# Kernel tuning notes

Measured on AMD Instinct MI355X. Metric: run time of the kernel, lower is better.

Reference implementation:

```python
import jax, jax.numpy as jnp
import numpy as np

NUM_GRAPHS = 100  # batch of graphs for pooling (dgl.max_nodes / WeightAndSum)


def _glorot(k, shape):
    lim = np.sqrt(6.0 / (shape[0] + shape[1])).astype(np.float32)
    return jax.random.uniform(k, shape, jnp.float32, -lim, lim)


def setup_inputs() -> dict:
    key = jax.random.key(0)
    ks = jax.random.split(key, 10)
    N, E, D, H = 100000, 1600000, 128, 128
    node_feats = jax.random.normal(ks[0], (N, D), dtype=jnp.float32)
    src = jax.random.randint(ks[1], (E,), 0, N, dtype=jnp.int32)
    dst = jax.random.randint(ks[2], (E,), 0, N, dtype=jnp.int32)
    graph_ids = jnp.sort(jax.random.randint(ks[3], (N,), 0, NUM_GRAPHS, dtype=jnp.int32))
    W1 = _glorot(ks[4], (D, H)); b1 = jnp.zeros((H,), jnp.float32)
    W2 = _glorot(ks[5], (H, H)); b2 = jnp.zeros((H,), jnp.float32)
    W3 = _glorot(ks[6], (H, H)); b3 = jnp.zeros((H,), jnp.float32)
    W_pool = _glorot(ks[7], (H, 1)); b_pool = jnp.zeros((1,), jnp.float32)
    return {"node_feats": node_feats, "src": src, "dst": dst, "graph_ids": graph_ids,
            "W1": W1, "b1": b1, "W2": W2, "b2": b2, "W3": W3, "b3": b3,
            "W_pool": W_pool, "b_pool": b_pool}


def _gcn_layer(h, W, b, src, dst, norm_src, norm_dst, N):
    # DGL GraphConv, norm='both': D_dst^{-1/2} (A^T (D_src^{-1/2} X W)) + b
    h = (h * norm_src[:, None]) @ W                      # [N, H]
    agg = jax.ops.segment_sum(h[src], dst, num_segments=N)  # gather + scatter-add
    return agg * norm_dst[:, None] + b


def reference(node_feats, src, dst, graph_ids, W1, b1, W2, b2, W3, b3, W_pool, b_pool):
    N = node_feats.shape[0]
    # dgl.add_self_loop (allow_zero_in_degree=False)
    loops = jnp.arange(N, dtype=src.dtype)
    src_sl = jnp.concatenate([src, loops])
    dst_sl = jnp.concatenate([dst, loops])
    ones = jnp.ones(src_sl.shape, jnp.float32)
    out_deg = jax.ops.segment_sum(ones, src_sl, num_segments=N)
    in_deg = jax.ops.segment_sum(ones, dst_sl, num_segments=N)
    norm_src = jax.lax.rsqrt(jnp.maximum(out_deg, 1.0))
    norm_dst = jax.lax.rsqrt(jnp.maximum(in_deg, 1.0))
    h = node_feats
    for W, b in ((W1, b1), (W2, b2), (W3, b3)):
        h = jax.nn.relu(_gcn_layer(h, W, b, src_sl, dst_sl, norm_src, norm_dst, N))
    # pooling_func: WeightAndSum (sigmoid-gated weighted sum per graph) + max_nodes
    w = jax.nn.sigmoid(h @ W_pool + b_pool)              # [N, 1]
    g_sum = jax.ops.segment_sum(h * w, graph_ids, num_segments=NUM_GRAPHS)
    g_max = jax.ops.segment_max(h, graph_ids, num_segments=NUM_GRAPHS)
    return jnp.concatenate([g_sum, g_max], axis=1)       # [G, 2H]
```

## Files before the change

### kernel.cpp

```cpp
#include <hip/hip_runtime.h>
#include <hip/hip_bf16.h>

#define DIM 128
#define CAP 64
#define NBMAX 64
#define BCAP 36864
#define CSPLIT 8

typedef __attribute__((ext_vector_type(8))) short bf16x8;
typedef __attribute__((ext_vector_type(4))) float f32x4;
typedef __bf16 bf16x2 __attribute__((ext_vector_type(2)));
union U16 { uint4 u; bf16x8 b; };
union UB { unsigned u; bf16x2 h; };

__device__ __forceinline__ unsigned short f2bf(float f) {
    unsigned u = __float_as_uint(f);
    unsigned r = (u + 0x7fffu + ((u >> 16) & 1u)) >> 16;
    return (unsigned short)r;
}
__device__ __forceinline__ unsigned pack2bf(float a, float b) {
    return (unsigned)f2bf(a) | ((unsigned)f2bf(b) << 16);
}
__device__ __forceinline__ float2 unpack2bf(unsigned v) {
    float2 r;
    r.x = __uint_as_float(v << 16);
    r.y = __uint_as_float(v & 0xffff0000u);
    return r;
}
__device__ __forceinline__ void accum8s(float* acc, uint4 v, float s) {
    float2 f0 = unpack2bf(v.x), f1 = unpack2bf(v.y);
    float2 f2 = unpack2bf(v.z), f3 = unpack2bf(v.w);
    acc[0] += s * f0.x; acc[1] += s * f0.y; acc[2] += s * f1.x; acc[3] += s * f1.y;
    acc[4] += s * f2.x; acc[5] += s * f2.y; acc[6] += s * f3.x; acc[7] += s * f3.y;
}
__device__ __forceinline__ void accum8m(float* acc, uint4 v, float s) {
    UB w0, w1, w2, w3;
    w0.u = v.x; w1.u = v.y; w2.u = v.z; w3.u = v.w;
    acc[0] = fmaf((float)w0.h[0], s, acc[0]);
    acc[1] = fmaf((float)w0.h[1], s, acc[1]);
    acc[2] = fmaf((float)w1.h[0], s, acc[2]);
    acc[3] = fmaf((float)w1.h[1], s, acc[3]);
    acc[4] = fmaf((float)w2.h[0], s, acc[4]);
    acc[5] = fmaf((float)w2.h[1], s, acc[5]);
    acc[6] = fmaf((float)w3.h[0], s, acc[6]);
    acc[7] = fmaf((float)w3.h[1], s, acc[7]);
}

__global__ __launch_bounds__(256) void k_bin(const int* __restrict__ src,
                                             const int* __restrict__ dst, int E,
                                             unsigned* __restrict__ binD,
                                             unsigned short* __restrict__ binS,
                                             int* __restrict__ cntD,
                                             int* __restrict__ cntS, int NB, int binGrid,
                                             const float* __restrict__ W1,
                                             const float* __restrict__ W2,
                                             const float* __restrict__ W3,
                                             unsigned* __restrict__ wT1g,
                                             unsigned* __restrict__ wT2g,
                                             unsigned* __restrict__ wT3g) {
    __shared__ int hD[NBMAX], hS[NBMAX], bD[NBMAX], bS[NBMAX];
    int t = threadIdx.x;
    if ((int)blockIdx.x >= binGrid) {
        int w = blockIdx.x - binGrid;
        const float* Wsrc = (w == 0) ? W1 : (w == 1) ? W2 : W3;
        unsigned* wTg = (w == 0) ? wT1g : (w == 1) ? wT2g : wT3g;
        int n = t >> 1;
        int kp0 = (t & 1) * 32;
#pragma unroll
        for (int i = 0; i < 32; i++) {
            int kp = kp0 + i;
            wTg[n * 64 + kp] = pack2bf(Wsrc[(2 * kp) * DIM + n], Wsrc[(2 * kp + 1) * DIM + n]);
        }
        return;
    }
    if (t < NB) { hD[t] = 0; hS[t] = 0; }
    __syncthreads();
    int e0 = blockIdx.x * 1024 + t * 4;
    int s[4], d[4];
    bool v[4];
#pragma unroll
    for (int i = 0; i < 4; i++) {
        v[i] = (e0 + i) < E;
        s[i] = 0; d[i] = 0;
        if (v[i]) { s[i] = src[e0 + i]; d[i] = dst[e0 + i]; }
    }
#pragma unroll
    for (int i = 0; i < 4; i++) {
        if (v[i]) {
            atomicAdd(&hD[d[i] >> 11], 1);
            atomicAdd(&hS[s[i] >> 11], 1);
        }
    }
    __syncthreads();
    if (t < NB) {
        bD[t] = atomicAdd(&cntD[t], hD[t]);
        bS[t] = atomicAdd(&cntS[t], hS[t]);
        hD[t] = 0; hS[t] = 0;
    }
    __syncthreads();
#pragma unroll
    for (int i = 0; i < 4; i++) {
        if (v[i]) {
            int bd = d[i] >> 11;
            int r = atomicAdd(&hD[bd], 1);
            int idx = bD[bd] + r;
            if (idx < BCAP)
                binD[bd * BCAP + idx] = ((unsigned)(d[i] & 2047) << 17) | (unsigned)s[i];
            int bs = s[i] >> 11;
            int r2 = atomicAdd(&hS[bs], 1);
            int idx2 = bS[bs] + r2;
            if (idx2 < BCAP) binS[bs * BCAP + idx2] = (unsigned short)(s[i] & 2047);
        }
    }
}

__global__ __launch_bounds__(256) void k_mega(const unsigned* __restrict__ binD,
                                              const unsigned short* __restrict__ binS,
                                              const int* __restrict__ cntD,
                                              const int* __restrict__ cntS,
                                              int* __restrict__ in_cnt,
                                              int* __restrict__ out_cnt,
                                              int* __restrict__ csr_pad,
                                              const float* __restrict__ x,
                                              const unsigned* __restrict__ wT1g,
                                              unsigned* __restrict__ xwb, int N,
                                              int NB) {
    __shared__ __align__(16) char smem[34816];
    int bid = blockIdx.x;
    int t = threadIdx.x;

    if (bid < NB * CSPLIT) {
        int b = bid / CSPLIT;
        int sub = bid - b * CSPLIT;
        int* h = (int*)smem;
        int* bArr = ((int*)smem) + 2048;
        for (int j = t; j < 2048; j += 256) h[j] = 0;
        __syncthreads();
        int base = b << 11;
        int nE = cntD[b];
        if (nE > BCAP) nE = BCAP;
        int chunk = (nE + CSPLIT - 1) / CSPLIT;
        int i0 = sub * chunk;
        int i1 = i0 + chunk;
        if (i1 > nE) i1 = nE;
        const unsigned* bb = &binD[b * BCAP];
        for (int i = i0 + t * 4; i < i1; i += 1024) {
            unsigned e[4];
            int k = i1 - i;
            if (k > 4) k = 4;
#pragma unroll
            for (int j = 0; j < 4; j++)
                if (j < k) e[j] = bb[i + j];
#pragma unroll
            for (int j = 0; j < 4; j++)
                if (j < k) atomicAdd(&h[e[j] >> 17], 1);
        }
        __syncthreads();
        for (int j = t; j < 2048; j += 256) {
            int hv = h[j];
            bArr[j] = hv ? atomicAdd(&in_cnt[base + j], hv) : 0;
            h[j] = 0;
        }
        __syncthreads();
        for (int i = i0 + t * 4; i < i1; i += 1024) {
            unsigned e[4];
            int k = i1 - i;
            if (k > 4) k = 4;
#pragma unroll
            for (int j = 0; j < 4; j++)
                if (j < k) e[j] = bb[i + j];
#pragma unroll
            for (int j = 0; j < 4; j++)
                if (j < k) {
                    int dl = (int)(e[j] >> 17);
                    int pos = bArr[dl] + atomicAdd(&h[dl], 1);
                    if (pos < CAP)
                        csr_pad[(size_t)(base + dl) * CAP + pos] = (int)(e[j] & 0x1FFFFu);
                }
        }
        return;
    }
    if (bid < 2 * NB * CSPLIT) {
        int bb2 = bid - NB * CSPLIT;
        int b = bb2 / CSPLIT;
        int sub = bb2 - b * CSPLIT;
        int* hist = (int*)smem;
        for (int j = t; j < 2048; j += 256) hist[j] = 0;
        __syncthreads();
        int base = b << 11;
        int nE = cntS[b];
        if (nE > BCAP) nE = BCAP;
        int chunk = (nE + CSPLIT - 1) / CSPLIT;
        int i0 = sub * chunk;
        int i1 = i0 + chunk;
        if (i1 > nE) i1 = nE;
        const unsigned short* bs = &binS[b * BCAP];
        for (int i = i0 + t * 4; i < i1; i += 1024) {
            unsigned short e[4];
            int k = i1 - i;
            if (k > 4) k = 4;
#pragma unroll
            for (int j = 0; j < 4; j++)
                if (j < k) e[j] = bs[i + j];
#pragma unroll
            for (int j = 0; j < 4; j++)
                if (j < k) atomicAdd(&hist[(int)e[j]], 1);
        }
        __syncthreads();
        for (int j = t; j < 2048; j += 256) {
            int hv = hist[j];
            if (hv) atomicAdd(&out_cnt[base + j], hv);
        }
        return;
    }
    int gb = bid - 2 * NB * CSPLIT;
    unsigned* wT = (unsigned*)smem;
#pragma unroll
    for (int i = 0; i < 8; i++) {
        int idx = t + i * 256;
        int row = idx >> 4;
        int col = idx & 15;
        *(uint4*)&wT[row * 68 + col * 4] = ((const uint4*)wT1g)[idx];
    }
    __syncthreads();
    int wave = t >> 6, lane = t & 63;
    int quad = lane >> 4, c = lane & 15;
    int m = gb * 64 + wave * 16 + c;
    bool mv = m < N;
    f32x4 acc[8];
#pragma unroll
    for (int i = 0; i < 8; i++) acc[i] = (f32x4){0.f, 0.f, 0.f, 0.f};

#pragma unroll
    for (int ks = 0; ks < 4; ks++) {
        U16 av;
        if (mv) {
            const float4* xr = (const float4*)&x[(size_t)m * DIM + ks * 32 + quad * 8];
            float4 f0 = xr[0], f1 = xr[1];
            av.u.x = pack2bf(f0.x, f0.y);
            av.u.y = pack2bf(f0.z, f0.w);
            av.u.z = pack2bf(f1.x, f1.y);
            av.u.w = pack2bf(f1.z, f1.w);
        } else {
            av.u = make_uint4(0, 0, 0, 0);
        }
#pragma unroll
        for (int cb = 0; cb < 8; cb++) {
            U16 bv;
            bv.u = *(const uint4*)&wT[(cb * 16 + c) * 68 + ks * 16 + quad * 4];
            acc[cb] = __builtin_amdgcn_mfma_f32_16x16x32_bf16(av.b, bv.b, acc[cb], 0, 0, 0);
        }
    }
    int rowBase = gb * 64 + wave * 16 + quad * 4;
#pragma unroll
    for (int r = 0; r < 4; r++) {
        int rowN = rowBase + r;
#pragma unroll
        for (int cb = 0; cb < 8; cb++) {
            float v = acc[cb][r];
            float vn = __shfl_xor(v, 1, 64);
            if (((c & 1) == 0) && rowN < N)
                xwb[rowN * 64 + cb * 8 + (c >> 1)] = pack2bf(v, vn);
        }
    }
}

__global__ __launch_bounds__(256) void k_nrm(const int* __restrict__ out_cnt,
                                             float* __restrict__ nsv, int N) {
    int i = (blockIdx.x * 256 + threadIdx.x) * 4;
    if (i + 3 < N) {
        int4 d = *(const int4*)&out_cnt[i];
        float4 r;
        r.x = rsqrtf((float)(d.x + 1));
        r.y = rsqrtf((float)(d.y + 1));
        r.z = rsqrtf((float)(d.z + 1));
        r.w = rsqrtf((float)(d.w + 1));
        *(float4*)&nsv[i] = r;
    } else {
        for (int j = i; j < N && j < i + 4; j++) nsv[j] = rsqrtf((float)(out_cnt[j] + 1));
    }
}

template <int MODE>
__device__ __forceinline__ void agg_body(const uint4* __restrict__ xwb4,
                                         const int* __restrict__ in_cnt,
                                         const int* __restrict__ csr_pad,
                                         const float* __restrict__ nsv,
                                         const float* __restrict__ bias,
                                         uint4* __restrict__ hb4,
                                         const float* __restrict__ Wp,
                                         const float* __restrict__ bp,
                                         float* __restrict__ wg, int N) {
    int wid = (blockIdx.x * 256 + threadIdx.x) >> 6;
    int lane = threadIdx.x & 63;
    int g = lane >> 4, c = lane & 15;
    int n = wid * 4 + g;
    bool nv = n < N;
    int deg_true = nv ? in_cnt[n] : 0;
    int deg = deg_true > CAP ? CAP : deg_true;
    float ndv = rsqrtf((float)(deg_true + 1));
    const int* row = csr_pad + (size_t)n * CAP;

    float acc[8];
#pragma unroll
    for (int i = 0; i < 8; i++) acc[i] = 0.f;

    if (nv) {
        float s0 = (MODE == 0) ? nsv[n] : ndv;
        accum8m(acc, xwb4[(size_t)n * 16 + c], s0);
    }
    for (int p = 0; p < deg; p += 4) {
        int sidx[4];
        uint4 gv[4];
        float sc[4];
        bool pv[4];
#pragma unroll
        for (int u = 0; u < 4; u++) {
            pv[u] = (p + u) < deg;
            sidx[u] = pv[u] ? row[p + u] : row[p];
        }
#pragma unroll
        for (int u = 0; u < 4; u++) gv[u] = xwb4[(size_t)sidx[u] * 16 + c];
#pragma unroll
        for (int u = 0; u < 4; u++) sc[u] = (MODE == 0) ? nsv[sidx[u]] : ndv;
#pragma unroll
        for (int u = 0; u < 4; u++)
            if (pv[u]) accum8m(acc, gv[u], sc[u]);
    }

    float mul = (MODE == 0) ? ndv : 1.f;
    float4 b0 = ((const float4*)bias)[2 * c];
    float4 b1 = ((const float4*)bias)[2 * c + 1];
    float o[8];
    o[0] = fmaxf(acc[0] * mul + b0.x, 0.f);
    o[1] = fmaxf(acc[1] * mul + b0.y, 0.f);
    o[2] = fmaxf(acc[2] * mul + b0.z, 0.f);
    o[3] = fmaxf(acc[3] * mul + b0.w, 0.f);
    o[4] = fmaxf(acc[4] * mul + b1.x, 0.f);
    o[5] = fmaxf(acc[5] * mul + b1.y, 0.f);
    o[6] = fmaxf(acc[6] * mul + b1.z, 0.f);
    o[7] = fmaxf(acc[7] * mul + b1.w, 0.f);
    if (nv) {
        uint4 w;
        w.x = pack2bf(o[0], o[1]);
        w.y = pack2bf(o[2], o[3]);
        w.z = pack2bf(o[4], o[5]);
        w.w = pack2bf(o[6], o[7]);
        hb4[(size_t)n * 16 + c] = w;
    }
    if (MODE == 2) {
        float4 w0 = ((const float4*)Wp)[2 * c];
        float4 w1 = ((const float4*)Wp)[2 * c + 1];
        float s = o[0] * w0.x + o[1] * w0.y + o[2] * w0.z + o[3] * w0.w +
                  o[4] * w1.x + o[5] * w1.y + o[6] * w1.z + o[7] * w1.w;
        s += __shfl_xor(s, 1, 64);
        s += __shfl_xor(s, 2, 64);
        s += __shfl_xor(s, 4, 64);
        s += __shfl_xor(s, 8, 64);
        if (nv && c == 0) wg[n] = 1.f / (1.f + expf(-(s + bp[0])));
    }
}

__global__ __launch_bounds__(256) void k_agg1(const uint4* __restrict__ xwb4,
                                              const int* __restrict__ in_cnt,
                                              const int* __restrict__ csr_pad,
                                              const float* __restrict__ nsv,
                                              const float* __restrict__ bias,
                                              uint4* __restrict__ hb4, int N) {
    agg_body<0>(xwb4, in_cnt, csr_pad, nsv, bias, hb4, nullptr, nullptr, nullptr, N);
}

__global__ __launch_bounds__(256) void k_agg(const uint4* __restrict__ xwb4,
                                             const int* __restrict__ in_cnt,
                                             const int* __restrict__ csr_pad,
                                             const float* __restrict__ bias,
                                             uint4* __restrict__ hb4, int N) {
    agg_body<1>(xwb4, in_cnt, csr_pad, nullptr, bias, hb4, nullptr, nullptr, nullptr, N);
}

__global__ __launch_bounds__(256) void k_agg_gate(const uint4* __restrict__ xwb4,
                                                  const int* __restrict__ in_cnt,
                                                  const int* __restrict__ csr_pad,
                                                  const float* __restrict__ bias,
                                                  uint4* __restrict__ hb4,
                                                  const float* __restrict__ Wp,
                                                  const float* __restrict__ bp,
                                                  float* __restrict__ wg, int N) {
    agg_body<2>(xwb4, in_cnt, csr_pad, nullptr, bias, hb4, Wp, bp, wg, N);
}

__global__ __launch_bounds__(256) void k_xw_mfma(const unsigned* __restrict__ hb,
                                                 const int* __restrict__ out_cnt,
                                                 const unsigned* __restrict__ wTg,
                                                 unsigned* __restrict__ xwb, int N) {
    __shared__ unsigned wT[128 * 68];
    int t = threadIdx.x;
#pragma unroll
    for (int i = 0; i < 8; i++) {
        int idx = t + i * 256;
        int row = idx >> 4;
        int col = idx & 15;
        *(uint4*)&wT[row * 68 + col * 4] = ((const uint4*)wTg)[idx];
    }
    __syncthreads();
    int wave = t >> 6, lane = t & 63;
    int quad = lane >> 4, c = lane & 15;
    int m = blockIdx.x * 64 + wave * 16 + c;
    bool mv = m < N;
    f32x4 acc[8];
#pragma unroll
    for (int i = 0; i < 8; i++) acc[i] = (f32x4){0.f, 0.f, 0.f, 0.f};

#pragma unroll
    for (int ks = 0; ks < 4; ks++) {
        U16 av;
        if (mv) av.u = *(const uint4*)&hb[m * 64 + ks * 16 + quad * 4];
        else av.u = make_uint4(0, 0, 0, 0);
#pragma unroll
        for (int cb = 0; cb < 8; cb++) {
            U16 bv;
            bv.u = *(const uint4*)&wT[(cb * 16 + c) * 68 + ks * 16 + quad * 4];
            acc[cb] = __builtin_amdgcn_mfma_f32_16x16x32_bf16(av.b, bv.b, acc[cb], 0, 0, 0);
        }
    }
    int rowBase = blockIdx.x * 64 + wave * 16 + quad * 4;
#pragma unroll
    for (int r = 0; r < 4; r++) {
        int rowN = rowBase + r;
        float nrm = (rowN < N) ? rsqrtf((float)(out_cnt[rowN] + 1)) : 0.f;
#pragma unroll
        for (int cb = 0; cb < 8; cb++) {
            float v = acc[cb][r] * nrm;
            float vn = __shfl_xor(v, 1, 64);
            if (((c & 1) == 0) && rowN < N)
                xwb[rowN * 64 + cb * 8 + (c >> 1)] = pack2bf(v, vn);
        }
    }
}

__device__ __forceinline__ int lower_bound(const int* a, int n, int key) {
    int lo = 0, hi = n;
    while (lo < hi) {
        int m = (lo + hi) >> 1;
        if (a[m] < key) lo = m + 1;
        else hi = m;
    }
    return lo;
}

__global__ __launch_bounds__(64) void k_pool(const unsigned* __restrict__ hb,
                                             const float* __restrict__ wg,
                                             const int* __restrict__ gids,
                                             float* __restrict__ out, int N) {
    int g = blockIdx.x >> 4;
    int part = blockIdx.x & 15;
    int t = threadIdx.x;
    int start = lower_bound(gids, N, g);
    int end = lower_bound(gids, N, g + 1);
    float2 sum = {0.f, 0.f}, mx = {0.f, 0.f};
    for (int n = start + part; n < end; n += 16) {
        float w = wg[n];
        float2 v = unpack2bf(hb[n * 64 + t]);
        sum.x += v.x * w;
        sum.y += v.y * w;
        mx.x = fmaxf(mx.x, v.x);
        mx.y = fmaxf(mx.y, v.y);
    }
    atomicAdd(&out[g * 256 + 2 * t], sum.x);
    atomicAdd(&out[g * 256 + 2 * t + 1], sum.y);
    atomicMax((int*)&out[g * 256 + 128 + 2 * t], __float_as_int(mx.x));
    atomicMax((int*)&out[g * 256 + 128 + 2 * t + 1], __float_as_int(mx.y));
}

extern "C" void kernel_launch(void* const* d_in, const int* in_sizes, int n_in,
                              void* d_out, int out_size, void* d_ws, size_t ws_size,
                              hipStream_t stream) {
    const float* node_feats = (const float*)d_in[0];
    const int* src = (const int*)d_in[1];
    const int* dst = (const int*)d_in[2];
    const int* gids = (const int*)d_in[3];
    const float* W1 = (const float*)d_in[4];
    const float* b1 = (const float*)d_in[5];
    const float* W2 = (const float*)d_in[6];
    const float* b2 = (const float*)d_in[7];
    const float* W3 = (const float*)d_in[8];
    const float* b3 = (const float*)d_in[9];
    const float* Wp = (const float*)d_in[10];
    const float* bp = (const float*)d_in[11];
    float* out = (float*)d_out;

    const int N = in_sizes[3];
    const int E = in_sizes[1];
    const int G = out_size / 256;
    const int NB = (N + 2047) >> 11;

    char* ws = (char*)d_ws;
    size_t o = 0;
    int* cntD = (int*)(ws + o);          o += NBMAX * 4;
    int* cntS = (int*)(ws + o);          o += NBMAX * 4;
    int* in_cnt = (int*)(ws + o);        o += (size_t)N * 4;
    int* out_cnt = (int*)(ws + o);       o += (size_t)N * 4;
    size_t zero_bytes = o;
    float* wg = (float*)(ws + o);        o += (size_t)N * 4;
    float* nsv = (float*)(ws + o);       o += (size_t)N * 4;
    o = (o + 15) & ~15ull;
    unsigned* wT1g = (unsigned*)(ws + o); o += 8192 * 4;
    unsigned* wT2g = (unsigned*)(ws + o); o += 8192 * 4;
    unsigned* wT3g = (unsigned*)(ws + o); o += 8192 * 4;
    unsigned* binD = (unsigned*)(ws + o); o += (size_t)NBMAX * BCAP * 4;
    unsigned short* binS = (unsigned short*)(ws + o); o += (size_t)NBMAX * BCAP * 2;
    o = (o + 15) & ~15ull;
    int* csr_pad = (int*)(ws + o);       o += (size_t)N * CAP * 4;
    unsigned* xwb = (unsigned*)(ws + o); o += (size_t)N * 64 * 4;
    unsigned* hb = (unsigned*)(ws + o);  o += (size_t)N * 64 * 4;
    (void)ws_size;

    (void)hipMemsetAsync(d_ws, 0, zero_bytes, stream);
    (void)hipMemsetAsync(d_out, 0, (size_t)out_size * 4, stream);

    int binGrid = (E + 1023) / 1024;
    int mmGrid = (N + 63) / 64;
    int aggGrid = (N + 15) / 16;
    int nrmGrid = (N + 1023) / 1024;

    k_bin<<<binGrid + 3, 256, 0, stream>>>(src, dst, E, binD, binS, cntD, cntS, NB, binGrid,
                                           W1, W2, W3, wT1g, wT2g, wT3g);
    k_mega<<<2 * NB * CSPLIT + mmGrid, 256, 0, stream>>>(binD, binS, cntD, cntS, in_cnt,
                                                         out_cnt, csr_pad, node_feats,
                                                         wT1g, xwb, N, NB);
    k_nrm<<<nrmGrid, 256, 0, stream>>>(out_cnt, nsv, N);
    k_agg1<<<aggGrid, 256, 0, stream>>>((const uint4*)xwb, in_cnt, csr_pad, nsv, b1,
                                        (uint4*)hb, N);
    k_xw_mfma<<<mmGrid, 256, 0, stream>>>(hb, out_cnt, wT2g, xwb, N);
    k_agg<<<aggGrid, 256, 0, stream>>>((const uint4*)xwb, in_cnt, csr_pad, b2,
                                       (uint4*)hb, N);
    k_xw_mfma<<<mmGrid, 256, 0, stream>>>(hb, out_cnt, wT3g, xwb, N);
    k_agg_gate<<<aggGrid, 256, 0, stream>>>((const uint4*)xwb, in_cnt, csr_pad, b3,
                                            (uint4*)hb, Wp, bp, wg, N);
    k_pool<<<G * 16, 64, 0, stream>>>(hb, wg, gids, out, N);
}
```

Measured before the change: 456.4 us.

## Slice XW features into 8 column planes for cache-friendly gather aggregation

The XW producer now writes features as 8 column-slice planes of 16 bf16 values each, and the aggregation kernels process one slice per block, with 4 lanes splitting each node's neighbor list and merging partials by shuffle. The aim is to shrink the working set of each gather pass so it fits in cache, making the random neighbor reads cheaper. In exchange there are 8x more blocks and redundant CSR index reads. The pooling gate is also split: partial dot products are accumulated with atomics and the sigmoid is applied in the pool kernel.

```diff
diff --git a/kernel.cpp b/kernel.cpp
--- a/kernel.cpp
+++ b/kernel.cpp
@@ -26,12 +26,6 @@
     r.x = __uint_as_float(v << 16);
     r.y = __uint_as_float(v & 0xffff0000u);
     return r;
-}
-__device__ __forceinline__ void accum8s(float* acc, uint4 v, float s) {
-    float2 f0 = unpack2bf(v.x), f1 = unpack2bf(v.y);
-    float2 f2 = unpack2bf(v.z), f3 = unpack2bf(v.w);
-    acc[0] += s * f0.x; acc[1] += s * f0.y; acc[2] += s * f1.x; acc[3] += s * f1.y;
-    acc[4] += s * f2.x; acc[5] += s * f2.y; acc[6] += s * f3.x; acc[7] += s * f3.y;
 }
 __device__ __forceinline__ void accum8m(float* acc, uint4 v, float s) {
     UB w0, w1, w2, w3;
@@ -260,7 +254,7 @@
             float v = acc[cb][r];
             float vn = __shfl_xor(v, 1, 64);
             if (((c & 1) == 0) && rowN < N)
-                xwb[rowN * 64 + cb * 8 + (c >> 1)] = pack2bf(v, vn);
+                xwb[(size_t)cb * N * 8 + (size_t)rowN * 8 + (c >> 1)] = pack2bf(v, vn);
         }
     }
 }
@@ -282,55 +276,68 @@
 }
 
 template <int MODE>
-__device__ __forceinline__ void agg_body(const uint4* __restrict__ xwb4,
+__device__ __forceinline__ void agg_body(const uint4* __restrict__ in4s,
                                          const int* __restrict__ in_cnt,
                                          const int* __restrict__ csr_pad,
                                          const float* __restrict__ nsv,
                                          const float* __restrict__ bias,
-                                         uint4* __restrict__ hb4,
+                                         uint4* __restrict__ out4,
                                          const float* __restrict__ Wp,
-                                         const float* __restrict__ bp,
-                                         float* __restrict__ wg, int N) {
-    int wid = (blockIdx.x * 256 + threadIdx.x) >> 6;
-    int lane = threadIdx.x & 63;
-    int g = lane >> 4, c = lane & 15;
-    int n = wid * 4 + g;
-    bool nv = n < N;
-    int deg_true = nv ? in_cnt[n] : 0;
+                                         float* __restrict__ wgp, int N) {
+    int f = blockIdx.x & 7;
+    int chunk = blockIdx.x >> 3;
+    int t = threadIdx.x;
+    int lane = t & 63;
+    int node_g = lane >> 3;
+    int slot = (lane >> 1) & 3;
+    int c2 = lane & 1;
+    int n0 = chunk * 32 + (t >> 6) * 8 + node_g;
+    bool nv = n0 < N;
+    int n = nv ? n0 : 0;
+    int deg_true = in_cnt[n];
     int deg = deg_true > CAP ? CAP : deg_true;
     float ndv = rsqrtf((float)(deg_true + 1));
     const int* row = csr_pad + (size_t)n * CAP;
+    const uint4* sl = in4s + (size_t)f * N * 2;
 
     float acc[8];
 #pragma unroll
     for (int i = 0; i < 8; i++) acc[i] = 0.f;
 
-    if (nv) {
+    if (slot == 0) {
         float s0 = (MODE == 0) ? nsv[n] : ndv;
-        accum8m(acc, xwb4[(size_t)n * 16 + c], s0);
-    }
-    for (int p = 0; p < deg; p += 4) {
-        int sidx[4];
-        uint4 gv[4];
-        float sc[4];
-        bool pv[4];
-#pragma unroll
-        for (int u = 0; u < 4; u++) {
-            pv[u] = (p + u) < deg;
-            sidx[u] = pv[u] ? row[p + u] : row[p];
-        }
-#pragma unroll
-        for (int u = 0; u < 4; u++) gv[u] = xwb4[(size_t)sidx[u] * 16 + c];
-#pragma unroll
-        for (int u = 0; u < 4; u++) sc[u] = (MODE == 0) ? nsv[sidx[u]] : ndv;
-#pragma unroll
-        for (int u = 0; u < 4; u++)
-            if (pv[u]) accum8m(acc, gv[u], sc[u]);
-    }
-
+        accum8m(acc, sl[(size_t)n * 2 + c2], s0);
+    }
+    for (int p = 0; p < deg; p += 16) {
+        int e0 = p + slot, e1 = p + 4 + slot, e2 = p + 8 + slot, e3 = p + 12 + slot;
+        int i0 = row[e0], i1 = row[e1], i2 = row[e2], i3 = row[e3];
+        bool v0 = e0 < deg, v1 = e1 < deg, v2 = e2 < deg, v3 = e3 < deg;
+        int g0 = v0 ? i0 : n, g1 = v1 ? i1 : n, g2 = v2 ? i2 : n, g3 = v3 ? i3 : n;
+        uint4 q0 = sl[(size_t)g0 * 2 + c2];
+        uint4 q1 = sl[(size_t)g1 * 2 + c2];
+        uint4 q2 = sl[(size_t)g2 * 2 + c2];
+        uint4 q3 = sl[(size_t)g3 * 2 + c2];
+        float s0, s1, s2, s3;
+        if (MODE == 0) {
+            float a0 = nsv[g0], a1 = nsv[g1], a2 = nsv[g2], a3 = nsv[g3];
+            s0 = v0 ? a0 : 0.f; s1 = v1 ? a1 : 0.f; s2 = v2 ? a2 : 0.f; s3 = v3 ? a3 : 0.f;
+        } else {
+            s0 = v0 ? ndv : 0.f; s1 = v1 ? ndv : 0.f;
+            s2 = v2 ? ndv : 0.f; s3 = v3 ? ndv : 0.f;
+        }
+        accum8m(acc, q0, s0);
+        accum8m(acc, q1, s1);
+        accum8m(acc, q2, s2);
+        accum8m(acc, q3, s3);
+    }
+#pragma unroll
+    for (int i = 0; i < 8; i++) {
+        acc[i] += __shfl_xor(acc[i], 2, 64);
+        acc[i] += __shfl_xor(acc[i], 4, 64);
+    }
     float mul = (MODE == 0) ? ndv : 1.f;
-    float4 b0 = ((const float4*)bias)[2 * c];
-    float4 b1 = ((const float4*)bias)[2 * c + 1];
+    float4 b0 = ((const float4*)bias)[f * 4 + c2 * 2];
+    float4 b1 = ((const float4*)bias)[f * 4 + c2 * 2 + 1];
     float o[8];
     o[0] = fmaxf(acc[0] * mul + b0.x, 0.f);
     o[1] = fmaxf(acc[1] * mul + b0.y, 0.f);
@@ -340,53 +347,49 @@
     o[5] = fmaxf(acc[5] * mul + b1.y, 0.f);
     o[6] = fmaxf(acc[6] * mul + b1.z, 0.f);
     o[7] = fmaxf(acc[7] * mul + b1.w, 0.f);
-    if (nv) {
+    if (nv && slot == 0) {
         uint4 w;
         w.x = pack2bf(o[0], o[1]);
         w.y = pack2bf(o[2], o[3]);
         w.z = pack2bf(o[4], o[5]);
         w.w = pack2bf(o[6], o[7]);
-        hb4[(size_t)n * 16 + c] = w;
+        out4[(size_t)n * 16 + f * 2 + c2] = w;
     }
     if (MODE == 2) {
-        float4 w0 = ((const float4*)Wp)[2 * c];
-        float4 w1 = ((const float4*)Wp)[2 * c + 1];
+        float4 w0 = ((const float4*)Wp)[f * 4 + c2 * 2];
+        float4 w1 = ((const float4*)Wp)[f * 4 + c2 * 2 + 1];
         float s = o[0] * w0.x + o[1] * w0.y + o[2] * w0.z + o[3] * w0.w +
                   o[4] * w1.x + o[5] * w1.y + o[6] * w1.z + o[7] * w1.w;
         s += __shfl_xor(s, 1, 64);
-        s += __shfl_xor(s, 2, 64);
-        s += __shfl_xor(s, 4, 64);
-        s += __shfl_xor(s, 8, 64);
-        if (nv && c == 0) wg[n] = 1.f / (1.f + expf(-(s + bp[0])));
-    }
-}
-
-__global__ __launch_bounds__(256) void k_agg1(const uint4* __restrict__ xwb4,
+        if (nv && (lane & 7) == 0) atomicAdd(&wgp[n], s);
+    }
+}
+
+__global__ __launch_bounds__(256) void k_agg1(const uint4* __restrict__ in4s,
                                               const int* __restrict__ in_cnt,
                                               const int* __restrict__ csr_pad,
                                               const float* __restrict__ nsv,
                                               const float* __restrict__ bias,
-                                              uint4* __restrict__ hb4, int N) {
-    agg_body<0>(xwb4, in_cnt, csr_pad, nsv, bias, hb4, nullptr, nullptr, nullptr, N);
-}
-
-__global__ __launch_bounds__(256) void k_agg(const uint4* __restrict__ xwb4,
+                                              uint4* __restrict__ out4, int N) {
+    agg_body<0>(in4s, in_cnt, csr_pad, nsv, bias, out4, nullptr, nullptr, N);
+}
+
+__global__ __launch_bounds__(256) void k_agg(const uint4* __restrict__ in4s,
                                              const int* __restrict__ in_cnt,
                                              const int* __restrict__ csr_pad,
                                              const float* __restrict__ bias,
-                                             uint4* __restrict__ hb4, int N) {
-    agg_body<1>(xwb4, in_cnt, csr_pad, nullptr, bias, hb4, nullptr, nullptr, nullptr, N);
-}
-
-__global__ __launch_bounds__(256) void k_agg_gate(const uint4* __restrict__ xwb4,
+                                             uint4* __restrict__ out4, int N) {
+    agg_body<1>(in4s, in_cnt, csr_pad, nullptr, bias, out4, nullptr, nullptr, N);
+}
+
+__global__ __launch_bounds__(256) void k_agg_gate(const uint4* __restrict__ in4s,
                                                   const int* __restrict__ in_cnt,
                                                   const int* __restrict__ csr_pad,
                                                   const float* __restrict__ bias,
-                                                  uint4* __restrict__ hb4,
+                                                  uint4* __restrict__ out4,
                                                   const float* __restrict__ Wp,
-                                                  const float* __restrict__ bp,
-                                                  float* __restrict__ wg, int N) {
-    agg_body<2>(xwb4, in_cnt, csr_pad, nullptr, bias, hb4, Wp, bp, wg, N);
+                                                  float* __restrict__ wgp, int N) {
+    agg_body<2>(in4s, in_cnt, csr_pad, nullptr, bias, out4, Wp, wgp, N);
 }
 
 __global__ __launch_bounds__(256) void k_xw_mfma(const unsigned* __restrict__ hb,
@@ -433,7 +436,7 @@
             float v = acc[cb][r] * nrm;
             float vn = __shfl_xor(v, 1, 64);
             if (((c & 1) == 0) && rowN < N)
-                xwb[rowN * 64 + cb * 8 + (c >> 1)] = pack2bf(v, vn);
+                xwb[(size_t)cb * N * 8 + (size_t)rowN * 8 + (c >> 1)] = pack2bf(v, vn);
         }
     }
 }
@@ -449,7 +452,8 @@
 }
 
 __global__ __launch_bounds__(64) void k_pool(const unsigned* __restrict__ hb,
-                                             const float* __restrict__ wg,
+                                             const float* __restrict__ wgp,
+                                             const float* __restrict__ bp,
                                              const int* __restrict__ gids,
                                              float* __restrict__ out, int N) {
     int g = blockIdx.x >> 4;
@@ -457,9 +461,12 @@
     int t = threadIdx.x;
     int start = lower_bound(gids, N, g);
     int end = lower_bound(gids, N, g + 1);
+    float bp0 = bp[0];
     float2 sum = {0.f, 0.f}, mx = {0.f, 0.f};
     for (int n = start + part; n < end; n += 16) {
-        float w = wg[n];
+        float w = 0.f;
+        if (t == 0) w = 1.f / (1.f + expf(-(wgp[n] + bp0)));
+        w = __shfl(w, 0, 64);
         float2 v = unpack2bf(hb[n * 64 + t]);
         sum.x += v.x * w;
         sum.y += v.y * w;
@@ -500,8 +507,8 @@
     int* cntS = (int*)(ws + o);          o += NBMAX * 4;
     int* in_cnt = (int*)(ws + o);        o += (size_t)N * 4;
     int* out_cnt = (int*)(ws + o);       o += (size_t)N * 4;
+    float* wgp = (float*)(ws + o);       o += (size_t)N * 4;
     size_t zero_bytes = o;
-    float* wg = (float*)(ws + o);        o += (size_t)N * 4;
     float* nsv = (float*)(ws + o);       o += (size_t)N * 4;
     o = (o + 15) & ~15ull;
     unsigned* wT1g = (unsigned*)(ws + o); o += 8192 * 4;
@@ -520,7 +527,7 @@
 
     int binGrid = (E + 1023) / 1024;
     int mmGrid = (N + 63) / 64;
-    int aggGrid = (N + 15) / 16;
+    int aggGrid = ((N + 31) / 32) * 8;
     int nrmGrid = (N + 1023) / 1024;
 
     k_bin<<<binGrid + 3, 256, 0, stream>>>(src, dst, E, binD, binS, cntD, cntS, NB, binGrid,
@@ -536,6 +543,6 @@
                                        (uint4*)hb, N);
     k_xw_mfma<<<mmGrid, 256, 0, stream>>>(hb, out_cnt, wT3g, xwb, N);
     k_agg_gate<<<aggGrid, 256, 0, stream>>>((const uint4*)xwb, in_cnt, csr_pad, b3,
-                                            (uint4*)hb, Wp, bp, wg, N);
-    k_pool<<<G * 16, 64, 0, stream>>>(hb, wg, gids, out, N);
-}
+                                            (uint4*)hb, Wp, wgp, N);
+    k_pool<<<G * 16, 64, 0, stream>>>(hb, wgp, bp, gids, out, N);
+}
```

Result: slower. 604.3 us (+32.4%).
